# Performance work log

Hardware: AMD Instinct MI355X
Metric: run time of the kernel (lower is better)

Reference implementation:

```python
import jax, jax.numpy as jnp
import numpy as np

DN = ('NCH', 'OIH', 'NCH')


def _dsc(x, dwk, dwb, pwk, pwb, groups):
    # depthwise conv (VALID) + pointwise 1x1 conv, both with bias
    y = jax.lax.conv_general_dilated(x, dwk, (1,), 'VALID', dimension_numbers=DN,
                                     feature_group_count=groups) + dwb[None, :, None]
    y = jax.lax.conv_general_dilated(y, pwk, (1,), 'VALID', dimension_numbers=DN) + pwb[None, :, None]
    return y


def _icoh(x):
    # x: (b, c, L) -> iCOH adjacency (b, c, c)
    b, c, _ = x.shape
    f = jnp.fft.fft(x, axis=-1)                                  # (b,c,L) complex
    cps = f[:, :, None, :] * jnp.conj(f)[:, None, :, :]          # (b,c,c,L)
    num = jnp.mean(jnp.imag(cps), axis=-1)
    den = jnp.sqrt(jnp.mean(jnp.abs(cps), axis=-1) ** 2)
    adj = num / den
    return (adj * (1.0 - jnp.eye(c, dtype=adj.dtype))).astype(jnp.float32)


def _forward(x, se_w1, se_w2, dw_k1, dw_b1, pw_k1, pw_b1, dw_k2, dw_b2, pw_k2, pw_b2,
             dw_k3, dw_b3, pw_k3, pw_b3, gcn_w, gcn_b,
             w_r, wb_r, w_u, wb_u, w_c, wb_c, b_r, b_u, b_c):
    b, s, c, L = x.shape
    out_gru = w_r.shape[1]
    # Squeeze-and-Excitation over segment dim, then max over segments
    sq = x.mean(axis=(2, 3))                                     # (b,s)
    a = jax.nn.sigmoid(jax.nn.relu(sq @ se_w1) @ se_w2)          # (b,s)
    max_seg = (x * a[:, :, None, None]).max(axis=1)              # (b,c,L)
    adj = _icoh(max_seg)                                         # (b,c,c)

    def step(h, xt):                                             # h: (b*c,gru), xt: (b,c,L)
        d = _dsc(xt, dw_k1, dw_b1, pw_k1, pw_b1, c)
        d = _dsc(d, dw_k2, dw_b2, pw_k2, pw_b2, c)
        d = _dsc(d, dw_k3, dw_b3, pw_k3, pw_b3, c)               # (b,c,c)
        adj_t = jax.nn.sigmoid(d + adj)
        g = (jnp.einsum('bij,bjl->bil', adj_t, xt) @ gcn_w + gcn_b).reshape(b * c, -1)
        cat = jnp.concatenate([g, h], axis=-1)
        r = jax.nn.sigmoid(cat @ w_r + wb_r + b_r)
        u = jax.nn.sigmoid(cat @ w_u + wb_u + b_u)
        ct = jnp.tanh(jnp.concatenate([g, r * h], axis=-1) @ w_c + wb_c + b_c)
        h = u * h + (1.0 - u) * ct
        return h, None

    h0 = jnp.zeros((b * c, out_gru), x.dtype)
    hT, _ = jax.lax.scan(step, h0, jnp.swapaxes(x, 0, 1))        # scan over s
    return hT.reshape(b, c, out_gru)[:, -1, :]                   # (b, out_gru)


def setup_inputs():
    key = jax.random.key(0)
    b, s, c, L, gcn, gru = 64, 30, 62, 169, 64, 64
    ks = jax.random.split(key, 16)
    W = 0.05
    inp = {
        'x': jax.random.normal(ks[0], (b, s, c, L), jnp.float32),
        'se_w1': jax.random.normal(ks[1], (s, s // 2), jnp.float32) * W,
        'se_w2': jax.random.normal(ks[2], (s // 2, s), jnp.float32) * W,
        'dw_k1': jax.random.normal(ks[3], (c, 1, 64), jnp.float32) * W,
        'dw_b1': jnp.zeros((c,), jnp.float32),
        'pw_k1': jax.random.normal(ks[4], (c, c, 1), jnp.float32) * W,
        'pw_b1': jnp.zeros((c,), jnp.float32),
        'dw_k2': jax.random.normal(ks[5], (c, 1, 32), jnp.float32) * W,
        'dw_b2': jnp.zeros((c,), jnp.float32),
        'pw_k2': jax.random.normal(ks[6], (c, c, 1), jnp.float32) * W,
        'pw_b2': jnp.zeros((c,), jnp.float32),
        'dw_k3': jax.random.normal(ks[7], (c, 1, 14), jnp.float32) * W,
        'dw_b3': jnp.zeros((c,), jnp.float32),
        'pw_k3': jax.random.normal(ks[8], (c, c, 1), jnp.float32) * W,
        'pw_b3': jnp.zeros((c,), jnp.float32),
        'gcn_w': jax.random.normal(ks[9], (L, gcn), jnp.float32) * W,
        'gcn_b': jnp.zeros((gcn,), jnp.float32),
        'w_r': jax.random.normal(ks[10], (gcn + gru, gru), jnp.float32) * W,
        'wb_r': jnp.zeros((gru,), jnp.float32),
        'w_u': jax.random.normal(ks[11], (gcn + gru, gru), jnp.float32) * W,
        'wb_u': jnp.zeros((gru,), jnp.float32),
        'w_c': jax.random.normal(ks[12], (gcn + gru, gru), jnp.float32) * W,
        'wb_c': jnp.zeros((gru,), jnp.float32),
        'b_r': jnp.zeros((gru,), jnp.float32),
        'b_u': jnp.zeros((gru,), jnp.float32),
        'b_c': jnp.zeros((gru,), jnp.float32),
    }
    return inp


def reference(x, se_w1, se_w2, dw_k1, dw_b1, pw_k1, pw_b1, dw_k2, dw_b2, pw_k2, pw_b2,
              dw_k3, dw_b3, pw_k3, pw_b3, gcn_w, gcn_b,
              w_r, wb_r, w_u, wb_u, w_c, wb_c, b_r, b_u, b_c):
    return _forward(x, se_w1, se_w2, dw_k1, dw_b1, pw_k1, pw_b1, dw_k2, dw_b2, pw_k2, pw_b2,
                    dw_k3, dw_b3, pw_k3, pw_b3, gcn_w, gcn_b,
                    w_r, wb_r, w_u, wb_u, w_c, wb_c, b_r, b_u, b_c)
```

## Files before the change

### kernel.cpp

```cpp
#include <hip/hip_runtime.h>
#include <hip/hip_bf16.h>
#include <math.h>

#define Bb 64
#define Ss 30
#define Cc 62
#define Ll 169
#define CL (Cc*Ll)
#define GRU 64
#define HTAPS 108
#define KSPLIT 16
#define KSLICE 656

typedef __attribute__((ext_vector_type(8))) short short8;
typedef __attribute__((ext_vector_type(4))) float f32x4;

__device__ __forceinline__ unsigned short f2bf(float f)
{
    union { float f; unsigned int u; } v; v.f = f;
    unsigned int u = v.u + 0x7fffu + ((v.u >> 16) & 1u);
    return (unsigned short)(u >> 16);
}


__global__ __launch_bounds__(256) void k_misc(
    const float* __restrict__ pwk1, const float* __restrict__ pwb1, const float* __restrict__ dwb1,
    const float* __restrict__ dwk2, const float* __restrict__ dwb2,
    const float* __restrict__ pwk2, const float* __restrict__ pwb2,
    const float* __restrict__ dwk3, const float* __restrict__ dwb3,
    const float* __restrict__ pwk3, const float* __restrict__ pwb3,
    float* __restrict__ Gout, float* __restrict__ Ccst)
{
    __shared__ float s0[Cc], s1[Cc], s2[Cc], F[14], k2[32];
    const int blk = blockIdx.x, t = threadIdx.x;
    if (blk < Cc) {
        const int e = blk;
        if (t < Cc) { s0[t] = pwk3[61*Cc + t]; s1[t] = pwk2[t*Cc + e]; }
        if (t < 32) k2[t] = dwk2[e*32 + t];
        __syncthreads();
        if (t < 14) {
            float acc = 0.f;
            for (int f = 0; f < Cc; ++f) acc += s0[f] * s1[f] * dwk3[f*14 + t];
            F[t] = acc;
        }
        __syncthreads();
        if (t < 45) {
            float acc = 0.f;
            int t0 = t - 31; if (t0 < 0) t0 = 0;
            int t1 = t; if (t1 > 13) t1 = 13;
            for (int tt = t0; tt <= t1; ++tt) acc += F[tt] * k2[t - tt];
            Gout[e*45 + t] = acc;
        }
    } else {
        if (t < Cc) s0[t] = dwb1[t];
        __syncthreads();
        if (t < Cc) {
            float acc = pwb1[t];
            for (int c = 0; c < Cc; ++c) acc += pwk1[t*Cc + c] * s0[c];
            float sk = 0.f;
            for (int a = 0; a < 32; ++a) sk += dwk2[t*32 + a];
            s1[t] = acc * sk + dwb2[t];
        }
        __syncthreads();
        if (t < Cc) {
            float acc = pwb2[t];
            for (int e = 0; e < Cc; ++e) acc += pwk2[t*Cc + e] * s1[e];
            float sk = 0.f;
            for (int tt = 0; tt < 14; ++tt) sk += dwk3[t*14 + tt];
            s2[t] = acc * sk + dwb3[t];
        }
        __syncthreads();
        if (t < 64) {
            float v = (t < Cc) ? pwk3[61*Cc + t] * s2[t] : 0.f;
            for (int off = 32; off; off >>= 1) v += __shfl_down(v, off);
            if (t == 0) Ccst[0] = v + pwb3[61];
        }
    }
}

__global__ __launch_bounds__(128) void k_h1h(const float* __restrict__ pwk1, const float* __restrict__ dwk1,
                                             const float* __restrict__ Gin, float* __restrict__ Heff)
{
    __shared__ float p1c[Cc], H1[45], k1[64];
    int c = blockIdx.x, t = threadIdx.x;
    if (t < Cc) p1c[t] = pwk1[t*Cc + c];
    if (t >= 64 && t < 128) k1[t - 64] = dwk1[c*64 + (t - 64)];
    __syncthreads();
    if (t < 45) {
        float acc = 0.f;
        for (int e = 0; e < Cc; ++e) acc += p1c[e] * Gin[e*45 + t];
        H1[t] = acc;
    }
    __syncthreads();
    if (t < HTAPS) {
        float acc = 0.f;
        int s0 = t - 63; if (s0 < 0) s0 = 0;
        int s1 = t; if (s1 > 44) s1 = 44;
        for (int s = s0; s <= s1; ++s) acc += H1[s] * k1[t - s];
        Heff[c*HTAPS + t] = acc;
    }
}

__global__ __launch_bounds__(256) void k_gemm(const float* __restrict__ x,
                                              const float* __restrict__ Heff,
                                              float* __restrict__ P)
{
    __shared__ __align__(16) unsigned short Xs[64*64];
    __shared__ __align__(16) unsigned short Hs[64*64];
    const int tid = threadIdx.x;
    const int mt = blockIdx.x % 30;
    const int ks = blockIdx.x / 30;
    const int k0 = ks * KSLICE;
    const int kend = (k0 + KSLICE < CL) ? (k0 + KSLICE) : CL;
    const int m0g = mt * 64;
    const int w = tid >> 6, l = tid & 63;
    const int arow = w*16 + (l & 15);
    const int klane = (l >> 4) * 8;
    const int sr = tid >> 2, sq4 = (tid & 3) << 4;

    f32x4 acc[4];
#pragma unroll
    for (int ct = 0; ct < 4; ++ct) acc[ct] = (f32x4){0.f, 0.f, 0.f, 0.f};

    for (int kb = k0; kb < kend; kb += 64) {
        {
            const float* xp = x + (size_t)(m0g + sr)*CL + kb + sq4;
            unsigned short tb[16];
            if (kb + 64 <= kend) {
#pragma unroll
                for (int t2 = 0; t2 < 8; ++t2) {
                    float2 v = *reinterpret_cast<const float2*>(xp + 2*t2);
                    tb[2*t2]   = f2bf(v.x);
                    tb[2*t2+1] = f2bf(v.y);
                }
            } else {
#pragma unroll
                for (int t = 0; t < 16; ++t) {
                    int col = kb + sq4 + t;
                    tb[t] = f2bf((col < kend) ? xp[t] : 0.f);
                }
            }
            int i0 = (sr*64 + sq4)     ^ ((sr & 7) << 3);
            int i1 = (sr*64 + sq4 + 8) ^ ((sr & 7) << 3);
            short8 p0, p1;
#pragma unroll
            for (int t = 0; t < 8; ++t) { p0[t] = (short)tb[t]; p1[t] = (short)tb[t+8]; }
            *reinterpret_cast<short8*>(&Xs[i0]) = p0;
            *reinterpret_cast<short8*>(&Xs[i1]) = p1;
        }
        {
            int j = sr;
            unsigned short tb[16];
#pragma unroll
            for (int t = 0; t < 16; ++t) {
                int kg = kb + sq4 + t;
                float hv = 0.f;
                if (kg < kend && j < Cc) {
                    int c = kg / Ll, ll = kg - c*Ll;
                    int a = ll - j;
                    if (a >= 0 && a < HTAPS) hv = Heff[c*HTAPS + a];
                }
                tb[t] = f2bf(hv);
            }
            int i0 = (j*64 + sq4)     ^ ((j & 7) << 3);
            int i1 = (j*64 + sq4 + 8) ^ ((j & 7) << 3);
            short8 p0, p1;
#pragma unroll
            for (int t = 0; t < 8; ++t) { p0[t] = (short)tb[t]; p1[t] = (short)tb[t+8]; }
            *reinterpret_cast<short8*>(&Hs[i0]) = p0;
            *reinterpret_cast<short8*>(&Hs[i1]) = p1;
        }
        __syncthreads();
#pragma unroll
        for (int ks2 = 0; ks2 < 2; ++ks2) {
            int kk0 = ks2*32 + klane;
            int ia = (arow*64 + kk0) ^ ((arow & 7) << 3);
            short8 af = *reinterpret_cast<const short8*>(&Xs[ia]);
#pragma unroll
            for (int ct = 0; ct < 4; ++ct) {
                int bcol = ct*16 + (l & 15);
                int ib = (bcol*64 + kk0) ^ ((bcol & 7) << 3);
                short8 bf = *reinterpret_cast<const short8*>(&Hs[ib]);
                acc[ct] = __builtin_amdgcn_mfma_f32_16x16x32_bf16(af, bf, acc[ct], 0, 0, 0);
            }
        }
        __syncthreads();
    }
#pragma unroll
    for (int ct = 0; ct < 4; ++ct) {
        int col = ct*16 + (l & 15);
        if (col < Cc) {
#pragma unroll
            for (int i = 0; i < 4; ++i) {
                int row = m0g + w*16 + (l >> 4)*4 + i;
                P[(size_t)(ks*1920 + row)*Cc + col] = acc[ct][i];
            }
        }
    }
}

__global__ __launch_bounds__(256) void k_g(const float* __restrict__ x, const float* __restrict__ P,
    const float* __restrict__ Ccst,
    const float* __restrict__ gcn_w, const float* __restrict__ gcn_b,
    const float* __restrict__ w_r, const float* __restrict__ w_u, const float* __restrict__ w_c,
    float* __restrict__ preR, float* __restrict__ preU, float* __restrict__ preC)
{
    __shared__ float adjt[Cc];
    __shared__ float v[Ll];
    __shared__ float g[GRU];
    int bt = blockIdx.x, t = bt >> 6, b = bt & 63;
    int m = b * Ss + t;
    int tid = threadIdx.x;
    if (tid < Cc) {
        float sv = Ccst[0];
#pragma unroll
        for (int ks = 0; ks < KSPLIT; ++ks) sv += P[((size_t)ks*1920 + m)*Cc + tid];
        adjt[tid] = 1.f / (1.f + expf(-sv));
    }
    __syncthreads();
    if (tid < Ll) {
        const float* xp = x + (size_t)m*CL + tid;
        float acc = 0.f;
        for (int j = 0; j < Cc; ++j) acc += adjt[j] * xp[j*Ll];
        v[tid] = acc;
    }
    __syncthreads();
    if (tid < GRU) {
        float acc = gcn_b[tid];
        for (int l = 0; l < Ll; ++l) acc += v[l] * gcn_w[l*GRU + tid];
        g[tid] = acc;
    }
    __syncthreads();
    if (tid < GRU) {
        float ar = 0.f, au = 0.f, ac = 0.f;
        for (int i = 0; i < GRU; ++i) {
            float gi = g[i];
            ar += gi * w_r[i*GRU + tid];
            au += gi * w_u[i*GRU + tid];
            ac += gi * w_c[i*GRU + tid];
        }
        preR[(size_t)bt*GRU + tid] = ar;
        preU[(size_t)bt*GRU + tid] = au;
        preC[(size_t)bt*GRU + tid] = ac;
    }
}

__global__ __launch_bounds__(256) void k_gru(const float* __restrict__ preR, const float* __restrict__ preU,
    const float* __restrict__ preC,
    const float* __restrict__ w_r, const float* __restrict__ wb_r,
    const float* __restrict__ w_u, const float* __restrict__ wb_u,
    const float* __restrict__ w_c, const float* __restrict__ wb_c,
    const float* __restrict__ b_r, const float* __restrict__ b_u, const float* __restrict__ b_c,
    float* __restrict__ out)
{
    __shared__ float h[GRU], rh[GRU];
    __shared__ float part[3][4][GRU];
    __shared__ float preS[Ss][3][GRU];
    const int b = blockIdx.x;
    const int t = threadIdx.x, o = t & 63, q = t >> 6;

    float wr[16], wu[16], wc[16];
#pragma unroll
    for (int i = 0; i < 16; ++i) {
        wr[i] = w_r[(GRU + q*16 + i)*GRU + o];
        wu[i] = w_u[(GRU + q*16 + i)*GRU + o];
        wc[i] = w_c[(GRU + q*16 + i)*GRU + o];
    }
    for (int u = t; u < Ss*GRU; u += 256) {
        int s = u >> 6, oo = u & 63;
        size_t base = (size_t)(s*Bb + b)*GRU + oo;
        preS[s][0][oo] = preR[base];
        preS[s][1][oo] = preU[base];
        preS[s][2][oo] = preC[base];
    }
    const float cr = wb_r[o] + b_r[o];
    const float cu = wb_u[o] + b_u[o];
    const float cc = wb_c[o] + b_c[o];
    if (t < GRU) h[t] = 0.f;
    float ug = 0.f;
    __syncthreads();

    for (int s = 0; s < Ss; ++s) {
        float ar = 0.f, au = 0.f;
#pragma unroll
        for (int i = 0; i < 16; ++i) {
            float hi = h[q*16 + i];
            ar += hi * wr[i];
            au += hi * wu[i];
        }
        part[0][q][o] = ar;
        part[1][q][o] = au;
        __syncthreads();
        if (q == 0) {
            float arf = preS[s][0][o] + cr + part[0][0][o] + part[0][1][o] + part[0][2][o] + part[0][3][o];
            float auf = preS[s][1][o] + cu + part[1][0][o] + part[1][1][o] + part[1][2][o] + part[1][3][o];
            float r = 1.f / (1.f + expf(-arf));
            ug = 1.f / (1.f + expf(-auf));
            rh[o] = r * h[o];
        }
        __syncthreads();
        float ac = 0.f;
#pragma unroll
        for (int i = 0; i < 16; ++i) ac += rh[q*16 + i] * wc[i];
        part[2][q][o] = ac;
        __syncthreads();
        if (q == 0) {
            float acf = preS[s][2][o] + cc + part[2][0][o] + part[2][1][o] + part[2][2][o] + part[2][3][o];
            float ct = tanhf(acf);
            float hn = ug * h[o] + (1.f - ug) * ct;
            h[o] = hn;
            if (s == Ss - 1) out[b*GRU + o] = hn;
        }
        __syncthreads();
    }
}

extern "C" void kernel_launch(void* const* d_in, const int* in_sizes, int n_in,
                              void* d_out, int out_size, void* d_ws, size_t ws_size,
                              hipStream_t stream)
{
    const float* x     = (const float*)d_in[0];
    const float* dwk1  = (const float*)d_in[3];
    const float* dwb1  = (const float*)d_in[4];
    const float* pwk1  = (const float*)d_in[5];
    const float* pwb1  = (const float*)d_in[6];
    const float* dwk2  = (const float*)d_in[7];
    const float* dwb2  = (const float*)d_in[8];
    const float* pwk2  = (const float*)d_in[9];
    const float* pwb2  = (const float*)d_in[10];
    const float* dwk3  = (const float*)d_in[11];
    const float* dwb3  = (const float*)d_in[12];
    const float* pwk3  = (const float*)d_in[13];
    const float* pwb3  = (const float*)d_in[14];
    const float* gcn_w = (const float*)d_in[15];
    const float* gcn_b = (const float*)d_in[16];
    const float* w_r   = (const float*)d_in[17];
    const float* wb_r  = (const float*)d_in[18];
    const float* w_u   = (const float*)d_in[19];
    const float* wb_u  = (const float*)d_in[20];
    const float* w_c   = (const float*)d_in[21];
    const float* wb_c  = (const float*)d_in[22];
    const float* b_r   = (const float*)d_in[23];
    const float* b_u   = (const float*)d_in[24];
    const float* b_c   = (const float*)d_in[25];
    float* out = (float*)d_out;

    float* ws   = (float*)d_ws;
    float* P    = ws;
    float* preR = P    + 1904640;
    float* preU = preR + 122880;
    float* preC = preU + 122880;
    float* Heff = preC + 122880;
    float* Ccst = Heff + 6696;
    float* Gbuf = Ccst + 8;

    k_misc<<<Cc + 1, 256, 0, stream>>>(pwk1, pwb1, dwb1, dwk2, dwb2, pwk2, pwb2,
                                       dwk3, dwb3, pwk3, pwb3, Gbuf, Ccst);
    k_h1h<<<Cc, 128, 0, stream>>>(pwk1, dwk1, Gbuf, Heff);
    k_gemm<<<30*KSPLIT, 256, 0, stream>>>(x, Heff, P);
    k_g<<<Ss*Bb, 256, 0, stream>>>(x, P, Ccst, gcn_w, gcn_b, w_r, w_u, w_c, preR, preU, preC);
    k_gru<<<Bb, 256, 0, stream>>>(preR, preU, preC, w_r, wb_r, w_u, wb_u, w_c, wb_c,
                                  b_r, b_u, b_c, out);
}
```

Baseline: 89.34 us.

## Precompute banded bf16 weight matrix and fuse prep kernels, double K-split

Merges the two small preprocessing kernels into one that also materialises the banded Toeplitz weight matrix as a bf16 array padded to whole 64-wide tiles. The GEMM then loads B tiles with plain vector loads instead of per-element index math, divisions and bounds checks. The K-split is doubled and tiles are divided evenly across splits to raise the block count. The cost is a larger partial-sum buffer that the downstream kernel must reduce, plus extra global traffic to write and read the expanded matrix. The fused prep kernel also recomputes the shared F/G intermediates redundantly in every block.

```diff
diff --git a/kernel.cpp b/kernel.cpp
--- a/kernel.cpp
+++ b/kernel.cpp
@@ -9,8 +9,9 @@
 #define CL (Cc*Ll)
 #define GRU 64
 #define HTAPS 108
-#define KSPLIT 16
-#define KSLICE 656
+#define KSPLIT 32
+#define NTILES 164
+#define HBS 10496
 
 typedef __attribute__((ext_vector_type(8))) short short8;
 typedef __attribute__((ext_vector_type(4))) float f32x4;
@@ -23,40 +24,27 @@
 }
 
 
-__global__ __launch_bounds__(256) void k_misc(
-    const float* __restrict__ pwk1, const float* __restrict__ pwb1, const float* __restrict__ dwb1,
+__global__ __launch_bounds__(256) void k_prep(
+    const float* __restrict__ dwk1, const float* __restrict__ dwb1,
+    const float* __restrict__ pwk1, const float* __restrict__ pwb1,
     const float* __restrict__ dwk2, const float* __restrict__ dwb2,
     const float* __restrict__ pwk2, const float* __restrict__ pwb2,
     const float* __restrict__ dwk3, const float* __restrict__ dwb3,
     const float* __restrict__ pwk3, const float* __restrict__ pwb3,
-    float* __restrict__ Gout, float* __restrict__ Ccst)
-{
-    __shared__ float s0[Cc], s1[Cc], s2[Cc], F[14], k2[32];
-    const int blk = blockIdx.x, t = threadIdx.x;
-    if (blk < Cc) {
-        const int e = blk;
-        if (t < Cc) { s0[t] = pwk3[61*Cc + t]; s1[t] = pwk2[t*Cc + e]; }
-        if (t < 32) k2[t] = dwk2[e*32 + t];
-        __syncthreads();
-        if (t < 14) {
-            float acc = 0.f;
-            for (int f = 0; f < Cc; ++f) acc += s0[f] * s1[f] * dwk3[f*14 + t];
-            F[t] = acc;
-        }
-        __syncthreads();
-        if (t < 45) {
-            float acc = 0.f;
-            int t0 = t - 31; if (t0 < 0) t0 = 0;
-            int t1 = t; if (t1 > 13) t1 = 13;
-            for (int tt = t0; tt <= t1; ++tt) acc += F[tt] * k2[t - tt];
-            Gout[e*45 + t] = acc;
-        }
-    } else {
+    float* __restrict__ Ccst, unsigned short* __restrict__ HBt)
+{
+    const int c = blockIdx.x, t = threadIdx.x;
+    if (c == Cc) {
+        for (int u = t; u < 64*(HBS - CL); u += 256) {
+            int j = u / (HBS - CL), l = u % (HBS - CL);
+            HBt[(size_t)j*HBS + CL + l] = 0;
+        }
+        __shared__ float s0[Cc], s1[Cc], s2[Cc];
         if (t < Cc) s0[t] = dwb1[t];
         __syncthreads();
         if (t < Cc) {
             float acc = pwb1[t];
-            for (int c = 0; c < Cc; ++c) acc += pwk1[t*Cc + c] * s0[c];
+            for (int cc2 = 0; cc2 < Cc; ++cc2) acc += pwk1[t*Cc + cc2] * s0[cc2];
             float sk = 0.f;
             for (int a = 0; a < 32; ++a) sk += dwk2[t*32 + a];
             s1[t] = acc * sk + dwb2[t];
@@ -75,20 +63,33 @@
             for (int off = 32; off; off >>= 1) v += __shfl_down(v, off);
             if (t == 0) Ccst[0] = v + pwb3[61];
         }
-    }
-}
-
-__global__ __launch_bounds__(128) void k_h1h(const float* __restrict__ pwk1, const float* __restrict__ dwk1,
-                                             const float* __restrict__ Gin, float* __restrict__ Heff)
-{
-    __shared__ float p1c[Cc], H1[45], k1[64];
-    int c = blockIdx.x, t = threadIdx.x;
-    if (t < Cc) p1c[t] = pwk1[t*Cc + c];
-    if (t >= 64 && t < 128) k1[t - 64] = dwk1[c*64 + (t - 64)];
+        return;
+    }
+    __shared__ float q[Cc];
+    __shared__ float F[Cc*14];
+    __shared__ float G[Cc*45];
+    __shared__ float H1[45], hc[HTAPS];
+    if (t < Cc) q[t] = pwk3[61*Cc + t];
+    __syncthreads();
+    for (int u = t; u < Cc*14; u += 256) {
+        int e = u / 14, tt = u % 14;
+        float acc = 0.f;
+        for (int f = 0; f < Cc; ++f) acc += q[f] * pwk2[f*Cc + e] * dwk3[f*14 + tt];
+        F[u] = acc;
+    }
+    __syncthreads();
+    for (int u = t; u < Cc*45; u += 256) {
+        int e = u / 45, s = u % 45;
+        float acc = 0.f;
+        int t0 = s - 31; if (t0 < 0) t0 = 0;
+        int t1 = s; if (t1 > 13) t1 = 13;
+        for (int tt = t0; tt <= t1; ++tt) acc += F[e*14 + tt] * dwk2[e*32 + (s - tt)];
+        G[u] = acc;
+    }
     __syncthreads();
     if (t < 45) {
         float acc = 0.f;
-        for (int e = 0; e < Cc; ++e) acc += p1c[e] * Gin[e*45 + t];
+        for (int e = 0; e < Cc; ++e) acc += pwk1[e*Cc + c] * G[e*45 + t];
         H1[t] = acc;
     }
     __syncthreads();
@@ -96,13 +97,21 @@
         float acc = 0.f;
         int s0 = t - 63; if (s0 < 0) s0 = 0;
         int s1 = t; if (s1 > 44) s1 = 44;
-        for (int s = s0; s <= s1; ++s) acc += H1[s] * k1[t - s];
-        Heff[c*HTAPS + t] = acc;
+        for (int s = s0; s <= s1; ++s) acc += H1[s] * dwk1[c*64 + (t - s)];
+        hc[t] = acc;
+    }
+    __syncthreads();
+    for (int u = t; u < 64*Ll; u += 256) {
+        int j = u / Ll, l = u - j*Ll;
+        int a = l - j;
+        unsigned short v = 0;
+        if (a >= 0 && a < HTAPS) v = f2bf(hc[a]);
+        HBt[(size_t)j*HBS + c*Ll + l] = v;
     }
 }
 
 __global__ __launch_bounds__(256) void k_gemm(const float* __restrict__ x,
-                                              const float* __restrict__ Heff,
+                                              const unsigned short* __restrict__ HBt,
                                               float* __restrict__ P)
 {
     __shared__ __align__(16) unsigned short Xs[64*64];
@@ -110,8 +119,8 @@
     const int tid = threadIdx.x;
     const int mt = blockIdx.x % 30;
     const int ks = blockIdx.x / 30;
-    const int k0 = ks * KSLICE;
-    const int kend = (k0 + KSLICE < CL) ? (k0 + KSLICE) : CL;
+    const int t0 = (NTILES * ks) / KSPLIT;
+    const int t1 = (NTILES * (ks + 1)) / KSPLIT;
     const int m0g = mt * 64;
     const int w = tid >> 6, l = tid & 63;
     const int arow = w*16 + (l & 15);
@@ -122,11 +131,12 @@
 #pragma unroll
     for (int ct = 0; ct < 4; ++ct) acc[ct] = (f32x4){0.f, 0.f, 0.f, 0.f};
 
-    for (int kb = k0; kb < kend; kb += 64) {
+    for (int kt = t0; kt < t1; ++kt) {
+        const int kb = kt * 64;
         {
             const float* xp = x + (size_t)(m0g + sr)*CL + kb + sq4;
             unsigned short tb[16];
-            if (kb + 64 <= kend) {
+            if (kb + 64 <= CL) {
 #pragma unroll
                 for (int t2 = 0; t2 < 8; ++t2) {
                     float2 v = *reinterpret_cast<const float2*>(xp + 2*t2);
@@ -137,7 +147,7 @@
 #pragma unroll
                 for (int t = 0; t < 16; ++t) {
                     int col = kb + sq4 + t;
-                    tb[t] = f2bf((col < kend) ? xp[t] : 0.f);
+                    tb[t] = f2bf((col < CL) ? xp[t] : 0.f);
                 }
             }
             int i0 = (sr*64 + sq4)     ^ ((sr & 7) << 3);
@@ -149,24 +159,11 @@
             *reinterpret_cast<short8*>(&Xs[i1]) = p1;
         }
         {
-            int j = sr;
-            unsigned short tb[16];
-#pragma unroll
-            for (int t = 0; t < 16; ++t) {
-                int kg = kb + sq4 + t;
-                float hv = 0.f;
-                if (kg < kend && j < Cc) {
-                    int c = kg / Ll, ll = kg - c*Ll;
-                    int a = ll - j;
-                    if (a >= 0 && a < HTAPS) hv = Heff[c*HTAPS + a];
-                }
-                tb[t] = f2bf(hv);
-            }
-            int i0 = (j*64 + sq4)     ^ ((j & 7) << 3);
-            int i1 = (j*64 + sq4 + 8) ^ ((j & 7) << 3);
-            short8 p0, p1;
-#pragma unroll
-            for (int t = 0; t < 8; ++t) { p0[t] = (short)tb[t]; p1[t] = (short)tb[t+8]; }
+            const unsigned short* hp = HBt + (size_t)sr*HBS + kb + sq4;
+            short8 p0 = *reinterpret_cast<const short8*>(hp);
+            short8 p1 = *reinterpret_cast<const short8*>(hp + 8);
+            int i0 = (sr*64 + sq4)     ^ ((sr & 7) << 3);
+            int i1 = (sr*64 + sq4 + 8) ^ ((sr & 7) << 3);
             *reinterpret_cast<short8*>(&Hs[i0]) = p0;
             *reinterpret_cast<short8*>(&Hs[i1]) = p1;
         }
@@ -347,17 +344,15 @@
 
     float* ws   = (float*)d_ws;
     float* P    = ws;
-    float* preR = P    + 1904640;
+    float* preR = P    + 3809280;
     float* preU = preR + 122880;
     float* preC = preU + 122880;
-    float* Heff = preC + 122880;
-    float* Ccst = Heff + 6696;
-    float* Gbuf = Ccst + 8;
-
-    k_misc<<<Cc + 1, 256, 0, stream>>>(pwk1, pwb1, dwb1, dwk2, dwb2, pwk2, pwb2,
-                                       dwk3, dwb3, pwk3, pwb3, Gbuf, Ccst);
-    k_h1h<<<Cc, 128, 0, stream>>>(pwk1, dwk1, Gbuf, Heff);
-    k_gemm<<<30*KSPLIT, 256, 0, stream>>>(x, Heff, P);
+    float* Ccst = preC + 122880;
+    unsigned short* HBt = (unsigned short*)(Ccst + 8);
+
+    k_prep<<<Cc + 1, 256, 0, stream>>>(dwk1, dwb1, pwk1, pwb1, dwk2, dwb2, pwk2, pwb2,
+                                       dwk3, dwb3, pwk3, pwb3, Ccst, HBt);
+    k_gemm<<<30*KSPLIT, 256, 0, stream>>>(x, HBt, P);
     k_g<<<Ss*Bb, 256, 0, stream>>>(x, P, Ccst, gcn_w, gcn_b, w_r, w_u, w_c, preR, preU, preC);
     k_gru<<<Bb, 256, 0, stream>>>(preR, preU, preC, w_r, wb_r, w_u, wb_u, w_c, wb_c,
                                   b_r, b_u, b_c, out);
```

New measurement: 106.5 us. 19.2% more time.
